# Optimization experiments

Hardware: AMD Instinct MI355X
Metric: run time of the kernel (lower is better)

## Reference

```python
import jax, jax.numpy as jnp
import numpy as np

E, I, O = 8, 1024, 1024   # num_experts, in_features, out_features
B = 16                    # number of molecular systems (segments)
N = 16384                 # total rows (atoms * coeffs); sum(mole_sizes) == N


def setup_inputs() -> dict:
    key = jax.random.key(0)
    k1, k2, k3, k4 = jax.random.split(key, 4)
    scale = (1.0 / I) ** 0.5
    x = jax.random.normal(k1, (N, I), dtype=jnp.float32)
    # init_linear: uniform(-k, k) with k = sqrt(1/in_features)
    weights = scale * 2.0 * (jax.random.uniform(k2, (E, O, I), dtype=jnp.float32) - 0.5)
    bias = scale * 2.0 * (jax.random.uniform(k3, (O,), dtype=jnp.float32) - 0.5)
    expert_mixing_coefficients = jax.random.uniform(k4, (B, E), dtype=jnp.float32)
    # segment sizes per system; equal sizes summing exactly to N (static under jit)
    mole_sizes = jnp.full((B,), N // B, dtype=jnp.int32)
    return {
        "x": x,
        "weights": weights,
        "bias": bias,
        "expert_mixing_coefficients": expert_mixing_coefficients,
        "mole_sizes": mole_sizes,
    }


def reference(x, weights, bias, expert_mixing_coefficients, mole_sizes):
    # Original: W_b = einsum('eoi,be->bio', weights, coeff); then segment_mm
    # applies x_seg_b @ W_b for each row-segment b.  By linearity this equals
    # projecting x through each expert and mixing with per-row coefficients,
    # which avoids materializing [B, I, O] synthesized weights per segment
    # while computing identical math.
    n = x.shape[0]
    b = expert_mixing_coefficients.shape[0]
    seg_id = jnp.repeat(jnp.arange(b), mole_sizes, total_repeat_length=n)  # [N]
    ct = expert_mixing_coefficients[seg_id]                               # [N, E]
    proj = jnp.einsum('ni,eoi->neo', x, weights)                          # [N, E, O]
    y = jnp.einsum('neo,ne->no', proj, ct) + bias                         # [N, O]
    return y
```

## Files before the change

kernel.cpp:

```cpp
#include <hip/hip_runtime.h>
#include <hip/hip_bf16.h>
#include <stdint.h>

constexpr int E_NUM  = 8;
constexpr int I_DIM  = 1024;
constexpr int O_DIM  = 1024;
constexpr int B_SEG  = 16;
constexpr int N_ROWS = 16384;

constexpr int BM = 256, BN = 256, BK = 64;
constexpr int NT = I_DIM / BK;

typedef __bf16 bf16x8 __attribute__((ext_vector_type(8)));
typedef float  f32x4  __attribute__((ext_vector_type(4)));
typedef unsigned short ushortx8 __attribute__((ext_vector_type(8)));

#define AS1 __attribute__((address_space(1)))
#define AS3 __attribute__((address_space(3)))

__device__ __forceinline__ unsigned short f2bf(float f) {
    unsigned int u = __float_as_uint(f);
    u += 0x7fffu + ((u >> 16) & 1u);
    return (unsigned short)(u >> 16);
}

__global__ __launch_bounds__(256) void prep(const float* __restrict__ x,
                                            unsigned short* __restrict__ xb,
                                            const float* __restrict__ w,
                                            const float* __restrict__ coeff,
                                            unsigned short* __restrict__ wb) {
    __shared__ float sc[B_SEG * E_NUM];
    const int bid = blockIdx.x;
    const int tid = threadIdx.x;

    if (bid < 4096) {
        size_t idx = ((size_t)bid * 256 + tid) * 16;
        const float4* p = (const float4*)(x + idx);
        float4 v0 = p[0], v1 = p[1], v2 = p[2], v3 = p[3];
        ushortx8 o0, o1;
        o0[0] = f2bf(v0.x); o0[1] = f2bf(v0.y); o0[2] = f2bf(v0.z); o0[3] = f2bf(v0.w);
        o0[4] = f2bf(v1.x); o0[5] = f2bf(v1.y); o0[6] = f2bf(v1.z); o0[7] = f2bf(v1.w);
        o1[0] = f2bf(v2.x); o1[1] = f2bf(v2.y); o1[2] = f2bf(v2.z); o1[3] = f2bf(v2.w);
        o1[4] = f2bf(v3.x); o1[5] = f2bf(v3.y); o1[6] = f2bf(v3.z); o1[7] = f2bf(v3.w);
        *(ushortx8*)(xb + idx)     = o0;
        *(ushortx8*)(xb + idx + 8) = o1;
    } else {
        if (tid < B_SEG * E_NUM) sc[tid] = coeff[tid];
        __syncthreads();

        size_t idx = ((size_t)(bid - 4096) * 256 + tid) * 8;
        float4 wv0[E_NUM], wv1[E_NUM];
#pragma unroll
        for (int e = 0; e < E_NUM; e++) {
            const float4* p = (const float4*)(w + (size_t)e * O_DIM * I_DIM + idx);
            wv0[e] = p[0];
            wv1[e] = p[1];
        }

#pragma unroll
        for (int b = 0; b < B_SEG; b++) {
            float a[8] = {0,0,0,0,0,0,0,0};
#pragma unroll
            for (int e = 0; e < E_NUM; e++) {
                float c = sc[b * E_NUM + e];
                a[0] += c * wv0[e].x; a[1] += c * wv0[e].y;
                a[2] += c * wv0[e].z; a[3] += c * wv0[e].w;
                a[4] += c * wv1[e].x; a[5] += c * wv1[e].y;
                a[6] += c * wv1[e].z; a[7] += c * wv1[e].w;
            }
            ushortx8 o;
#pragma unroll
            for (int j = 0; j < 8; j++) o[j] = f2bf(a[j]);
            *(ushortx8*)(wb + (size_t)b * O_DIM * I_DIM + idx) = o;
        }
    }
}

__device__ __forceinline__ bf16x8 lds_read_b128(unsigned addr) {
    bf16x8 r;
    asm volatile("ds_read_b128 %0, %1" : "=v"(r) : "v"(addr));
    return r;
}

__global__ __launch_bounds__(512, 2) void gemm_moe(
    const unsigned short* __restrict__ xb,
    const unsigned short* __restrict__ wb,
    const float* __restrict__ bias,
    const int* __restrict__ msz,
    float* __restrict__ out)
{
    __shared__ __align__(16) char sLDS[131072];

    const int lid  = blockIdx.x;
    const int xcd  = lid & 7;
    const int idx  = lid >> 3;
    const int seg  = (xcd << 1) | (idx >> 4);
    const int t16  = idx & 15;
    const int mblk = t16 >> 2;
    const int nblk = t16 & 3;

    int off = 0;
    for (int b = 0; b < seg; b++) off += msz[b];
    const int row0 = off + mblk * BM;
    const int col0 = nblk * BN;
    const unsigned short* wseg = wb + (size_t)seg * O_DIM * I_DIM;

    const int tid  = threadIdx.x;
    const int wave = tid >> 6;
    const int lane = tid & 63;
    const int wr = wave >> 2, wc = wave & 3;
    const int quad = lane >> 4, l16 = lane & 15;

    const int srow8  = lane >> 3;
    const int schunk = (lane & 7) ^ srow8;
    const unsigned short* gA0 = xb   + (size_t)(row0 + wave * 8 + srow8) * I_DIM + schunk * 8;
    const unsigned short* gA1 = gA0 + (size_t)128 * I_DIM;
    const unsigned short* gB0 = wseg + (size_t)(col0 + wave * 8 + srow8) * I_DIM + schunk * 8;
    const unsigned short* gB1 = gB0 + (size_t)128 * I_DIM;

    const unsigned rdA0 = (unsigned)((wr * 16 + l16) * 128 + (((0 + quad) ^ (l16 & 7)) * 16));
    const unsigned rdA1 = (unsigned)((wr * 16 + l16) * 128 + (((4 + quad) ^ (l16 & 7)) * 16));
    const unsigned rdB0 = (unsigned)(65536 + (wc * 16 + l16) * 128 + (((0 + quad) ^ (l16 & 7)) * 16));
    const unsigned rdB1 = (unsigned)(65536 + (wc * 16 + l16) * 128 + (((4 + quad) ^ (l16 & 7)) * 16));

    bf16x8 af[4][2], bfr[2][2];
    f32x4 acc[8][4];
#pragma unroll
    for (int m = 0; m < 8; ++m)
#pragma unroll
        for (int n = 0; n < 4; ++n)
            acc[m][n] = (f32x4){0.f, 0.f, 0.f, 0.f};

#define LOAD_A(S) do { _Pragma("unroll") for (int mm = 0; mm < 4; ++mm) {           \
        af[mm][0] = lds_read_b128(rdA0 + (S) * 16384u + mm * 4096u);                \
        af[mm][1] = lds_read_b128(rdA1 + (S) * 16384u + mm * 4096u); } } while (0)
#define LOAD_B(S) do { _Pragma("unroll") for (int nn = 0; nn < 2; ++nn) {           \
        bfr[nn][0] = lds_read_b128(rdB0 + (S) * 16384u + nn * 8192u);               \
        bfr[nn][1] = lds_read_b128(rdB1 + (S) * 16384u + nn * 8192u); } } while (0)

#define STAGE_A(H, S, ST) do {                                                      \
        const unsigned short* g_ = ((H) ? gA1 : gA0) + (size_t)(ST) * 64;           \
        __builtin_amdgcn_global_load_lds((const AS1 void*)g_,                       \
            (AS3 void*)(sLDS + (S) * 16384 + wave * 1024), 16, 0, 0);               \
        __builtin_amdgcn_global_load_lds((const AS1 void*)(g_ + (size_t)64 * I_DIM),\
            (AS3 void*)(sLDS + (S) * 16384 + 8192 + wave * 1024), 16, 0, 0); } while (0)
#define STAGE_B(H, S, ST) do {                                                      \
        const unsigned short* g_ = ((H) ? gB1 : gB0) + (size_t)(ST) * 64;           \
        __builtin_amdgcn_global_load_lds((const AS1 void*)g_,                       \
            (AS3 void*)(sLDS + 65536 + (S) * 16384 + wave * 1024), 16, 0, 0);       \
        __builtin_amdgcn_global_load_lds((const AS1 void*)(g_ + (size_t)64 * I_DIM),\
            (AS3 void*)(sLDS + 65536 + (S) * 16384 + 8192 + wave * 1024), 16, 0, 0); } while (0)

#define MFMA_Q(MH, NH) do { _Pragma("unroll") for (int mm = 0; mm < 4; ++mm)        \
        _Pragma("unroll") for (int nn = 0; nn < 2; ++nn)                            \
        _Pragma("unroll") for (int kk = 0; kk < 2; ++kk)                            \
            acc[(MH) * 4 + mm][(NH) * 2 + nn] =                                     \
                __builtin_amdgcn_mfma_f32_16x16x32_bf16(af[mm][kk], bfr[nn][kk],    \
                    acc[(MH) * 4 + mm][(NH) * 2 + nn], 0, 0, 0); } while (0)

#define PH_MID() do { __builtin_amdgcn_s_barrier();                                 \
        asm volatile("s_waitcnt lgkmcnt(0)");                                       \
        __builtin_amdgcn_sched_barrier(0);                                          \
        __builtin_amdgcn_s_setprio(1); } while (0)
#define PH_END() do { __builtin_amdgcn_s_setprio(0);                                \
        __builtin_amdgcn_sched_barrier(0);                                          \
        __builtin_amdgcn_s_barrier(); } while (0)

#define TILE(RS0, RS1, SS01, SS23, ST1, ST2) do {                                   \
                                                                 \
        LOAD_A(RS0); LOAD_B(RS1); STAGE_A(1, SS01, ST1);                            \
        PH_MID(); MFMA_Q(0, 1); PH_END();                                           \
                                                                 \
        LOAD_B(RS0); STAGE_B(1, SS01, ST1);                                         \
        PH_MID(); MFMA_Q(0, 0); PH_END();                                           \
                                                 \
        LOAD_A(RS1); STAGE_A(0, SS23, ST2);                                         \
        PH_MID(); MFMA_Q(1, 0); PH_END();                                           \
                                                                 \
        LOAD_B(RS1); STAGE_B(0, SS23, ST2);                                         \
        PH_MID(); MFMA_Q(1, 1);                                                     \
        __builtin_amdgcn_s_setprio(0);                                              \
        __builtin_amdgcn_sched_barrier(0);                                          \
        asm volatile("s_waitcnt vmcnt(4)");                                         \
        __builtin_amdgcn_sched_barrier(0);                                          \
        __builtin_amdgcn_s_barrier();                                               \
    } while (0)

    STAGE_A(0, 0, 0); STAGE_B(0, 0, 0);
    STAGE_A(1, 1, 0); STAGE_B(1, 1, 0);
    STAGE_A(0, 2, 1); STAGE_B(0, 2, 1);
    asm volatile("s_waitcnt vmcnt(4)");
    __builtin_amdgcn_sched_barrier(0);
    __builtin_amdgcn_s_barrier();

#pragma unroll 1
    for (int tp = 0; tp < 8; ++tp) {
        const int t0 = 2 * tp, t1 = t0 + 1;
        const int s1a = (t0 + 1 < 15) ? t0 + 1 : 15;
        const int s2a = (t0 + 2 < 15) ? t0 + 2 : 15;
        const int s1b = (t1 + 1 < 15) ? t1 + 1 : 15;
        const int s2b = (t1 + 2 < 15) ? t1 + 2 : 15;
        TILE(0, 1, 3, 0, s1a, s2a);
        TILE(2, 3, 1, 2, s1b, s2b);
    }

#undef TILE
#undef PH_END
#undef PH_MID
#undef MFMA_Q
#undef STAGE_B
#undef STAGE_A
#undef LOAD_B
#undef LOAD_A

    float bv[4];
#pragma unroll
    for (int n = 0; n < 4; ++n)
        bv[n] = bias[col0 + n * 64 + wc * 16 + l16];

#pragma unroll
    for (int m = 0; m < 8; ++m) {
#pragma unroll
        for (int r = 0; r < 4; ++r) {
            int row = row0 + m * 32 + wr * 16 + quad * 4 + r;
            float* po = out + (size_t)row * O_DIM + col0 + wc * 16 + l16;
#pragma unroll
            for (int n = 0; n < 4; ++n)
                po[n * 64] = acc[m][n][r] + bv[n];
        }
    }
}

extern "C" void kernel_launch(void* const* d_in, const int* in_sizes, int n_in,
                              void* d_out, int out_size, void* d_ws, size_t ws_size,
                              hipStream_t stream) {
    const float* x     = (const float*)d_in[0];
    const float* w     = (const float*)d_in[1];
    const float* bias  = (const float*)d_in[2];
    const float* coeff = (const float*)d_in[3];
    const int*   msz   = (const int*)d_in[4];
    float* out = (float*)d_out;

    unsigned short* xb = (unsigned short*)d_ws;
    unsigned short* wb = xb + (size_t)N_ROWS * I_DIM;

    prep<<<4096 + 512, 256, 0, stream>>>(x, xb, w, coeff, wb);

    gemm_moe<<<B_SEG * (1024 / BM) * (1024 / BN), 512, 0, stream>>>(xb, wb, bias, msz, out);
}
```

Measured before the change: 197.0 us.

## Restructure GEMM LDS pipeline with double-buffered fragments and split weight-prep blocks

The GEMM main loop now keeps two sets of A and B register fragments and reorders the four MFMA quadrants so each LDS read is reused across two quadrants. Global-to-LDS staging now runs one k-tile ahead instead of two, with vmcnt waits after most phases. The prep kernel places the weight-mixing blocks first and splits each one across two blocks of eight segments, which gives more parallelism on that heavier path. The extra fragment registers add pressure, and the shorter prefetch distance may expose more global-load latency.

```diff
diff --git a/kernel.cpp b/kernel.cpp
--- a/kernel.cpp
+++ b/kernel.cpp
@@ -33,8 +33,39 @@
     const int bid = blockIdx.x;
     const int tid = threadIdx.x;
 
-    if (bid < 4096) {
-        size_t idx = ((size_t)bid * 256 + tid) * 16;
+    if (bid < 1024) {
+        if (tid < B_SEG * E_NUM) sc[tid] = coeff[tid];
+        __syncthreads();
+
+        const int sb = (bid & 1) * 8;
+        size_t idx = ((size_t)(bid >> 1) * 256 + tid) * 8;
+        float4 wv0[E_NUM], wv1[E_NUM];
+#pragma unroll
+        for (int e = 0; e < E_NUM; e++) {
+            const float4* p = (const float4*)(w + (size_t)e * O_DIM * I_DIM + idx);
+            wv0[e] = p[0];
+            wv1[e] = p[1];
+        }
+
+#pragma unroll
+        for (int bq = 0; bq < 8; bq++) {
+            const int b = sb + bq;
+            float a[8] = {0,0,0,0,0,0,0,0};
+#pragma unroll
+            for (int e = 0; e < E_NUM; e++) {
+                float c = sc[b * E_NUM + e];
+                a[0] += c * wv0[e].x; a[1] += c * wv0[e].y;
+                a[2] += c * wv0[e].z; a[3] += c * wv0[e].w;
+                a[4] += c * wv1[e].x; a[5] += c * wv1[e].y;
+                a[6] += c * wv1[e].z; a[7] += c * wv1[e].w;
+            }
+            ushortx8 o;
+#pragma unroll
+            for (int j = 0; j < 8; j++) o[j] = f2bf(a[j]);
+            *(ushortx8*)(wb + (size_t)b * O_DIM * I_DIM + idx) = o;
+        }
+    } else {
+        size_t idx = ((size_t)(bid - 1024) * 256 + tid) * 16;
         const float4* p = (const float4*)(x + idx);
         float4 v0 = p[0], v1 = p[1], v2 = p[2], v3 = p[3];
         ushortx8 o0, o1;
@@ -44,35 +75,6 @@
         o1[4] = f2bf(v3.x); o1[5] = f2bf(v3.y); o1[6] = f2bf(v3.z); o1[7] = f2bf(v3.w);
         *(ushortx8*)(xb + idx)     = o0;
         *(ushortx8*)(xb + idx + 8) = o1;
-    } else {
-        if (tid < B_SEG * E_NUM) sc[tid] = coeff[tid];
-        __syncthreads();
-
-        size_t idx = ((size_t)(bid - 4096) * 256 + tid) * 8;
-        float4 wv0[E_NUM], wv1[E_NUM];
-#pragma unroll
-        for (int e = 0; e < E_NUM; e++) {
-            const float4* p = (const float4*)(w + (size_t)e * O_DIM * I_DIM + idx);
-            wv0[e] = p[0];
-            wv1[e] = p[1];
-        }
-
-#pragma unroll
-        for (int b = 0; b < B_SEG; b++) {
-            float a[8] = {0,0,0,0,0,0,0,0};
-#pragma unroll
-            for (int e = 0; e < E_NUM; e++) {
-                float c = sc[b * E_NUM + e];
-                a[0] += c * wv0[e].x; a[1] += c * wv0[e].y;
-                a[2] += c * wv0[e].z; a[3] += c * wv0[e].w;
-                a[4] += c * wv1[e].x; a[5] += c * wv1[e].y;
-                a[6] += c * wv1[e].z; a[7] += c * wv1[e].w;
-            }
-            ushortx8 o;
-#pragma unroll
-            for (int j = 0; j < 8; j++) o[j] = f2bf(a[j]);
-            *(ushortx8*)(wb + (size_t)b * O_DIM * I_DIM + idx) = o;
-        }
     }
 }
 
@@ -123,7 +125,7 @@
     const unsigned rdB0 = (unsigned)(65536 + (wc * 16 + l16) * 128 + (((0 + quad) ^ (l16 & 7)) * 16));
     const unsigned rdB1 = (unsigned)(65536 + (wc * 16 + l16) * 128 + (((4 + quad) ^ (l16 & 7)) * 16));
 
-    bf16x8 af[4][2], bfr[2][2];
+    bf16x8 af0[4][2], af1[4][2], b0[2][2], b1[2][2];
     f32x4 acc[8][4];
 #pragma unroll
     for (int m = 0; m < 8; ++m)
@@ -131,12 +133,12 @@
         for (int n = 0; n < 4; ++n)
             acc[m][n] = (f32x4){0.f, 0.f, 0.f, 0.f};
 
-#define LOAD_A(S) do { _Pragma("unroll") for (int mm = 0; mm < 4; ++mm) {           \
-        af[mm][0] = lds_read_b128(rdA0 + (S) * 16384u + mm * 4096u);                \
-        af[mm][1] = lds_read_b128(rdA1 + (S) * 16384u + mm * 4096u); } } while (0)
-#define LOAD_B(S) do { _Pragma("unroll") for (int nn = 0; nn < 2; ++nn) {           \
-        bfr[nn][0] = lds_read_b128(rdB0 + (S) * 16384u + nn * 8192u);               \
-        bfr[nn][1] = lds_read_b128(rdB1 + (S) * 16384u + nn * 8192u); } } while (0)
+#define LOAD_A(DST, S) do { _Pragma("unroll") for (int mm = 0; mm < 4; ++mm) {      \
+        DST[mm][0] = lds_read_b128(rdA0 + (S) * 16384u + mm * 4096u);               \
+        DST[mm][1] = lds_read_b128(rdA1 + (S) * 16384u + mm * 4096u); } } while (0)
+#define LOAD_B(DST, S) do { _Pragma("unroll") for (int nn = 0; nn < 2; ++nn) {      \
+        DST[nn][0] = lds_read_b128(rdB0 + (S) * 16384u + nn * 8192u);               \
+        DST[nn][1] = lds_read_b128(rdB1 + (S) * 16384u + nn * 8192u); } } while (0)
 
 #define STAGE_A(H, S, ST) do {                                                      \
         const unsigned short* g_ = ((H) ? gA1 : gA0) + (size_t)(ST) * 64;           \
@@ -151,44 +153,40 @@
         __builtin_amdgcn_global_load_lds((const AS1 void*)(g_ + (size_t)64 * I_DIM),\
             (AS3 void*)(sLDS + 65536 + (S) * 16384 + 8192 + wave * 1024), 16, 0, 0); } while (0)
 
-#define MFMA_Q(MH, NH) do { _Pragma("unroll") for (int mm = 0; mm < 4; ++mm)        \
+#define MFMA_Q(MH, NH, A, BV) do { _Pragma("unroll") for (int mm = 0; mm < 4; ++mm) \
         _Pragma("unroll") for (int nn = 0; nn < 2; ++nn)                            \
         _Pragma("unroll") for (int kk = 0; kk < 2; ++kk)                            \
             acc[(MH) * 4 + mm][(NH) * 2 + nn] =                                     \
-                __builtin_amdgcn_mfma_f32_16x16x32_bf16(af[mm][kk], bfr[nn][kk],    \
+                __builtin_amdgcn_mfma_f32_16x16x32_bf16(A[mm][kk], BV[nn][kk],      \
                     acc[(MH) * 4 + mm][(NH) * 2 + nn], 0, 0, 0); } while (0)
 
-#define PH_MID() do { __builtin_amdgcn_s_barrier();                                 \
+#define PH_MID() do { __builtin_amdgcn_sched_barrier(0);                            \
+        __builtin_amdgcn_s_barrier();                                               \
         asm volatile("s_waitcnt lgkmcnt(0)");                                       \
         __builtin_amdgcn_sched_barrier(0);                                          \
         __builtin_amdgcn_s_setprio(1); } while (0)
-#define PH_END() do { __builtin_amdgcn_s_setprio(0);                                \
+#define PH_END_W() do { __builtin_amdgcn_s_setprio(0);                              \
+        __builtin_amdgcn_sched_barrier(0);                                          \
+        asm volatile("s_waitcnt vmcnt(4)");                                         \
         __builtin_amdgcn_sched_barrier(0);                                          \
         __builtin_amdgcn_s_barrier(); } while (0)
-
-#define TILE(RS0, RS1, SS01, SS23, ST1, ST2) do {                                   \
-                                                                 \
-        LOAD_A(RS0); LOAD_B(RS1); STAGE_A(1, SS01, ST1);                            \
-        PH_MID(); MFMA_Q(0, 1); PH_END();                                           \
-                                                                 \
-        LOAD_B(RS0); STAGE_B(1, SS01, ST1);                                         \
-        PH_MID(); MFMA_Q(0, 0); PH_END();                                           \
-                                                 \
-        LOAD_A(RS1); STAGE_A(0, SS23, ST2);                                         \
-        PH_MID(); MFMA_Q(1, 0); PH_END();                                           \
-                                                                 \
-        LOAD_B(RS1); STAGE_B(0, SS23, ST2);                                         \
-        PH_MID(); MFMA_Q(1, 1);                                                     \
-        __builtin_amdgcn_s_setprio(0);                                              \
-        __builtin_amdgcn_sched_barrier(0);                                          \
-        asm volatile("s_waitcnt vmcnt(4)");                                         \
-        __builtin_amdgcn_sched_barrier(0);                                          \
-        __builtin_amdgcn_s_barrier();                                               \
+#define PH_END_N() do { __builtin_amdgcn_s_setprio(0);                              \
+        __builtin_amdgcn_sched_barrier(0);                                          \
+        __builtin_amdgcn_s_barrier(); } while (0)
+
+#define TILE(R0, R1, S0, S1, ST) do {                                               \
+        LOAD_A(af0, R0); LOAD_B(b0, R0); STAGE_A(0, S0, ST);                        \
+        PH_MID(); MFMA_Q(0, 0, af0, b0); PH_END_W();                                \
+        LOAD_A(af1, R1); STAGE_B(0, S0, ST);                                        \
+        PH_MID(); MFMA_Q(1, 0, af1, b0); PH_END_W();                                \
+        LOAD_B(b1, R1); STAGE_A(1, S1, ST);                                         \
+        PH_MID(); MFMA_Q(1, 1, af1, b1); PH_END_N();                                \
+        STAGE_B(1, S1, ST);                                                         \
+        PH_MID(); MFMA_Q(0, 1, af0, b1); PH_END_W();                                \
     } while (0)
 
     STAGE_A(0, 0, 0); STAGE_B(0, 0, 0);
     STAGE_A(1, 1, 0); STAGE_B(1, 1, 0);
-    STAGE_A(0, 2, 1); STAGE_B(0, 2, 1);
     asm volatile("s_waitcnt vmcnt(4)");
     __builtin_amdgcn_sched_barrier(0);
     __builtin_amdgcn_s_barrier();
@@ -196,16 +194,15 @@
 #pragma unroll 1
     for (int tp = 0; tp < 8; ++tp) {
         const int t0 = 2 * tp, t1 = t0 + 1;
-        const int s1a = (t0 + 1 < 15) ? t0 + 1 : 15;
-        const int s2a = (t0 + 2 < 15) ? t0 + 2 : 15;
-        const int s1b = (t1 + 1 < 15) ? t1 + 1 : 15;
-        const int s2b = (t1 + 2 < 15) ? t1 + 2 : 15;
-        TILE(0, 1, 3, 0, s1a, s2a);
-        TILE(2, 3, 1, 2, s1b, s2b);
+        const int st0 = (t0 + 1 < NT) ? t0 + 1 : NT - 1;
+        const int st1 = (t1 + 1 < NT) ? t1 + 1 : NT - 1;
+        TILE(0, 1, 2, 3, st0);
+        TILE(2, 3, 0, 1, st1);
     }
 
 #undef TILE
-#undef PH_END
+#undef PH_END_N
+#undef PH_END_W
 #undef PH_MID
 #undef MFMA_Q
 #undef STAGE_B
@@ -244,7 +241,7 @@
     unsigned short* xb = (unsigned short*)d_ws;
     unsigned short* wb = xb + (size_t)N_ROWS * I_DIM;
 
-    prep<<<4096 + 512, 256, 0, stream>>>(x, xb, w, coeff, wb);
+    prep<<<1024 + 4096, 256, 0, stream>>>(x, xb, w, coeff, wb);
 
     gemm_moe<<<B_SEG * (1024 / BM) * (1024 / BN), 512, 0, stream>>>(xb, wb, bias, msz, out);
 }
```

New measurement: 192.9 us. 2.1% less time.
